# Kernel optimization log

Measured on AMD Instinct MI355X. Metric: run time of the kernel, lower is better.

The kernel has to match this reference:

```python
import jax, jax.numpy as jnp
import numpy as np

B, H, N, D, E = 2, 8, 512, 16, 128  # batch, heads, nodes, qkv_dim, embedding_dim


def setup_inputs() -> dict:
    key = jax.random.key(0)
    ks = jax.random.split(key, 6)
    return {
        "q": jax.random.normal(ks[0], (B, H, N, D), dtype=jnp.float32),
        "k": jax.random.normal(ks[1], (B, H, N, D), dtype=jnp.float32),
        "v": jax.random.normal(ks[2], (B, H, N, D), dtype=jnp.float32),
        "z": jax.random.normal(ks[3], (B, N, N, E), dtype=jnp.float32),
        "Wz1": jax.random.normal(ks[4], (E, H * D), dtype=jnp.float32) * (1.0 / np.sqrt(E)),
        "Wz2": jax.random.normal(ks[5], (E, H * D), dtype=jnp.float32) * (1.0 / np.sqrt(E)),
    }


def _heads(zp, b, n, h):
    # [b, n, n, h*d] -> [b, h, n, n, d]
    return zp.reshape(b, n, n, h, -1).transpose(0, 3, 1, 2, 4)


def reference(q, k, v, z, Wz1, Wz2):
    b, h, n, d = q.shape
    z1 = _heads(z @ Wz1, b, n, h)  # bhnmd
    z2 = _heads(z @ Wz2, b, n, h)  # bhnmd
    # score = sum_d (q + z1) * (k + z2), expanded to avoid materializing qz/kz
    score = (jnp.einsum('bhnd,bhmd->bhnm', q, k)
             + jnp.einsum('bhnd,bhnmd->bhnm', q, z2)
             + jnp.einsum('bhnmd,bhmd->bhnm', z1, k)
             + jnp.einsum('bhnmd,bhnmd->bhnm', z1, z2))
    score = score / jnp.sqrt(jnp.asarray(d, dtype=score.dtype))
    weights = jax.nn.softmax(score, axis=-1)  # [b, h, n, m]
    out = jnp.einsum('bhnm,bhmd->bhnd', weights, v)
    return out.transpose(0, 2, 1, 3).reshape(b, n, h * d)
```

## Files before the change

kernel.cpp:

```cpp
#include <hip/hip_runtime.h>

constexpr int CB = 2;
constexpr int CH = 8;
constexpr int CN = 512;
constexpr int CD = 16;
constexpr int CE = 128;
constexpr int CHD = CH * CD;
constexpr int TM = 32;
constexpr int NTILE = CN / TM;
constexpr int NT = 512;

typedef __attribute__((ext_vector_type(8))) short short8;
typedef __attribute__((ext_vector_type(4))) float f32x4;

__device__ __forceinline__ unsigned short f2bf_rne(float x) {
  union { float f; unsigned int u; } a; a.f = x;
  unsigned int r = a.u + 0x7fffu + ((a.u >> 16) & 1u);
  return (unsigned short)(r >> 16);
}

__device__ __forceinline__ void split_pair(float x0, float x1,
                                           unsigned int& hi, unsigned int& lo) {
  unsigned int u0 = __float_as_uint(x0), u1 = __float_as_uint(x1);
  unsigned int h0 = u0 & 0xffff0000u, h1 = u1 & 0xffff0000u;
  float l0 = x0 - __uint_as_float(h0);
  float l1 = x1 - __uint_as_float(h1);
  hi = h1 | (u0 >> 16);
  lo = (__float_as_uint(l1) & 0xffff0000u) | (__float_as_uint(l0) >> 16);
}

__device__ __forceinline__ void split8(const float4 a, const float4 b,
                                       short8& hi, short8& lo) {
  union { unsigned int u[4]; short8 s; } H, L;
  split_pair(a.x, a.y, H.u[0], L.u[0]);
  split_pair(a.z, a.w, H.u[1], L.u[1]);
  split_pair(b.x, b.y, H.u[2], L.u[2]);
  split_pair(b.z, b.w, H.u[3], L.u[3]);
  hi = H.s; lo = L.s;
}

#define MFMA(A, B, C) __builtin_amdgcn_mfma_f32_16x16x32_bf16((A), (B), (C), 0, 0, 0)

__global__ __launch_bounds__(NT, 4) void fused_mixedscore_attn(
    const float* __restrict__ q, const float* __restrict__ kk,
    const float* __restrict__ v, const float* __restrict__ z,
    const float* __restrict__ W1, const float* __restrict__ W2,
    float* __restrict__ out)
{
  const int n = blockIdx.x;
  const int b = blockIdx.y;
  const int tid = threadIdx.x;
  const int lane = tid & 63;
  const int h = tid >> 6;
  const int col = lane & 15;
  const int quad = lane >> 4;

  __shared__ unsigned short zh[2][TM * CE];
  __shared__ unsigned short zl[2][TM * CE];

  const float* gz = z + (size_t)(b * CN + n) * CN * CE;

  const int sr = tid >> 4;
  const int sc = (tid & 15) * 8;
  const int wb = sr * 256 + ((sc * 2) ^ ((sr & 7) << 4));

  float4 zr0, zr1;
  {
    const float* g0 = gz + sr * CE + sc;
    zr0 = *(const float4*)(g0);
    zr1 = *(const float4*)(g0 + 4);
  }

  short8 B1[4], B2[4];
  {
    const int c = h * CD + col;
#pragma unroll
    for (int ks = 0; ks < 4; ++ks) {
      union { unsigned int u[4]; short8 s; } U1, U2;
#pragma unroll
      for (int jp = 0; jp < 4; ++jp) {
        const int e = ks * 32 + quad * 8 + jp * 2;
        const float a0 = W1[(size_t)e * CHD + c];
        const float a1 = W1[(size_t)(e + 1) * CHD + c];
        const float w0 = W2[(size_t)e * CHD + c];
        const float w1 = W2[(size_t)(e + 1) * CHD + c];
        U1.u[jp] = (unsigned int)f2bf_rne(a0) | ((unsigned int)f2bf_rne(a1) << 16);
        U2.u[jp] = (unsigned int)f2bf_rne(w0) | ((unsigned int)f2bf_rne(w1) << 16);
      }
      B1[ks] = U1.s;
      B2[ks] = U2.s;
    }
  }

  const float4 qv =
      *(const float4*)&q[((size_t)(b * CH + h) * CN + n) * CD + quad * 4];

  f32x4 Oa = f32x4{0.f, 0.f, 0.f, 0.f};
  float mrun = -3.0e38f;
  float srun = 0.f;

  for (int t = 0; t < NTILE; ++t) {
    const int cb = t & 1;
    const int m0 = t * TM;

    {
      short8 h8, l8;
      split8(zr0, zr1, h8, l8);
      *(short8*)((char*)&zh[cb][0] + wb) = h8;
      *(short8*)((char*)&zl[cb][0] + wb) = l8;
    }
    __syncthreads();

    if (t + 1 < NTILE) {
      const float* g1 = gz + ((size_t)(t + 1) * TM + sr) * CE + sc;
      zr0 = *(const float4*)(g1);
      zr1 = *(const float4*)(g1 + 4);
    }

    f32x4 acc1[2], acc2[2];
#pragma unroll
    for (int mt = 0; mt < 2; ++mt) {
      acc1[mt] = f32x4{0.f, 0.f, 0.f, 0.f};
      acc2[mt] = f32x4{0.f, 0.f, 0.f, 0.f};
    }

    const char* zhb = (const char*)&zh[cb][0];
    const char* zlb = (const char*)&zl[cb][0];
#pragma unroll
    for (int ks = 0; ks < 4; ++ks) {
#pragma unroll
      for (int mt = 0; mt < 2; ++mt) {
        const int row = mt * 16 + col;
        const int off = row * 256 + ((ks * 64 + quad * 16) ^ ((row & 7) << 4));
        const short8 ah = *(const short8*)(zhb + off);
        const short8 al = *(const short8*)(zlb + off);
        acc1[mt] = MFMA(B1[ks], ah, acc1[mt]);
        acc2[mt] = MFMA(B2[ks], ah, acc2[mt]);
        acc1[mt] = MFMA(B1[ks], al, acc1[mt]);
        acc2[mt] = MFMA(B2[ks], al, acc2[mt]);
      }
    }

    float sc2[2];
#pragma unroll
    for (int mt = 0; mt < 2; ++mt) {
      const int m = m0 + mt * 16 + col;
      const float4 k4 =
          *(const float4*)&kk[((size_t)(b * CH + h) * CN + m) * CD + quad * 4];
      float p = (qv.x + acc1[mt][0]) * (k4.x + acc2[mt][0]);
      p += (qv.y + acc1[mt][1]) * (k4.y + acc2[mt][1]);
      p += (qv.z + acc1[mt][2]) * (k4.z + acc2[mt][2]);
      p += (qv.w + acc1[mt][3]) * (k4.w + acc2[mt][3]);
      p += __shfl_xor(p, 16);
      p += __shfl_xor(p, 32);
      sc2[mt] = p * 0.25f;
    }

    {
      float tmax = fmaxf(sc2[0], sc2[1]);
      tmax = fmaxf(tmax, __shfl_xor(tmax, 1));
      tmax = fmaxf(tmax, __shfl_xor(tmax, 2));
      tmax = fmaxf(tmax, __shfl_xor(tmax, 4));
      tmax = fmaxf(tmax, __shfl_xor(tmax, 8));
      const float mnew = fmaxf(mrun, tmax);
      const float alpha = __expf(mrun - mnew);
      mrun = mnew;
      const float e0 = __expf(sc2[0] - mnew);
      const float e1 = __expf(sc2[1] - mnew);
      float ls = e0 + e1;
      ls += __shfl_xor(ls, 1);
      ls += __shfl_xor(ls, 2);
      ls += __shfl_xor(ls, 4);
      ls += __shfl_xor(ls, 8);
      srun = srun * alpha + ls;

      const float* vb = v + ((size_t)(b * CH + h) * CN) * CD + quad * 4;
      const float4 v0 = *(const float4*)&vb[(size_t)(m0 + col) * CD];
      const float4 v1 = *(const float4*)&vb[(size_t)(m0 + 16 + col) * CD];
      Oa[0] = Oa[0] * alpha + e0 * v0.x + e1 * v1.x;
      Oa[1] = Oa[1] * alpha + e0 * v0.y + e1 * v1.y;
      Oa[2] = Oa[2] * alpha + e0 * v0.z + e1 * v1.z;
      Oa[3] = Oa[3] * alpha + e0 * v0.w + e1 * v1.w;
    }
  }

#pragma unroll
  for (int rg = 0; rg < 4; ++rg) {
    float o = Oa[rg];
    o += __shfl_xor(o, 1);
    o += __shfl_xor(o, 2);
    o += __shfl_xor(o, 4);
    o += __shfl_xor(o, 8);
    Oa[rg] = o;
  }
  if (col == 0) {
    const float inv = 1.0f / srun;
    float4 o4;
    o4.x = Oa[0] * inv;
    o4.y = Oa[1] * inv;
    o4.z = Oa[2] * inv;
    o4.w = Oa[3] * inv;
    *(float4*)&out[(size_t)(b * CN + n) * CHD + h * CD + quad * 4] = o4;
  }
}

extern "C" void kernel_launch(void* const* d_in, const int* in_sizes, int n_in,
                              void* d_out, int out_size, void* d_ws, size_t ws_size,
                              hipStream_t stream) {
  const float* q  = (const float*)d_in[0];
  const float* kv = (const float*)d_in[1];
  const float* v  = (const float*)d_in[2];
  const float* z  = (const float*)d_in[3];
  const float* W1 = (const float*)d_in[4];
  const float* W2 = (const float*)d_in[5];
  float* out = (float*)d_out;
  (void)in_sizes; (void)n_in; (void)out_size; (void)d_ws; (void)ws_size;

  dim3 grid(CN, CB);
  hipLaunchKernelGGL(fused_mixedscore_attn, grid, dim3(NT), 0, stream,
                     q, kv, v, z, W1, W2, out);
}
```

Measured before the change: 376.8 us.

## Double m-tile size to 64 and prefetch k/v before the MFMA loop

Raises the z tile per iteration from 32 to 64 rows, so each thread stages 16 floats instead of 8 and each wave runs four m-subtiles per barrier. This halves the number of loop iterations and __syncthreads calls and gives more MFMA work per sync. k and v loads for the tile are also moved to the top of the iteration so their latency overlaps the LDS staging and MFMAs. In exchange, LDS use doubles (64 KB across the two buffers) and register pressure rises, which may reduce occupancy under launch_bounds(512,4).

New measurement: 404.0 us. 7.2% more time.

```diff
diff --git a/kernel.cpp b/kernel.cpp
--- a/kernel.cpp
+++ b/kernel.cpp
@@ -6,7 +6,7 @@
 constexpr int CD = 16;
 constexpr int CE = 128;
 constexpr int CHD = CH * CD;
-constexpr int TM = 32;
+constexpr int TM = 64;
 constexpr int NTILE = CN / TM;
 constexpr int NT = 512;
 
@@ -60,15 +60,18 @@
 
   const float* gz = z + (size_t)(b * CN + n) * CN * CE;
 
-  const int sr = tid >> 4;
-  const int sc = (tid & 15) * 8;
-  const int wb = sr * 256 + ((sc * 2) ^ ((sr & 7) << 4));
-
-  float4 zr0, zr1;
+  const int sr = tid >> 3;
+  const int sc = (tid & 7) * 16;
+  const int wb0 = sr * 256 + ((sc * 2) ^ ((sr & 7) << 4));
+  const int wb1 = sr * 256 + ((sc * 2 + 16) ^ ((sr & 7) << 4));
+
+  float4 zr0, zr1, zr2, zr3;
   {
     const float* g0 = gz + sr * CE + sc;
     zr0 = *(const float4*)(g0);
     zr1 = *(const float4*)(g0 + 4);
+    zr2 = *(const float4*)(g0 + 8);
+    zr3 = *(const float4*)(g0 + 12);
   }
 
   short8 B1[4], B2[4];
@@ -99,15 +102,31 @@
   float mrun = -3.0e38f;
   float srun = 0.f;
 
+  const float* kbase = kk + ((size_t)(b * CH + h) * CN) * CD + quad * 4;
+  const float* vbase = v + ((size_t)(b * CH + h) * CN) * CD + quad * 4;
+
   for (int t = 0; t < NTILE; ++t) {
     const int cb = t & 1;
     const int m0 = t * TM;
 
+    float4 k4[4], v4[4];
+#pragma unroll
+    for (int mt = 0; mt < 4; ++mt) {
+      const size_t m = (size_t)(m0 + mt * 16 + col) * CD;
+      k4[mt] = *(const float4*)&kbase[m];
+      v4[mt] = *(const float4*)&vbase[m];
+    }
+
     {
+      char* zhb = (char*)&zh[cb][0];
+      char* zlb = (char*)&zl[cb][0];
       short8 h8, l8;
       split8(zr0, zr1, h8, l8);
-      *(short8*)((char*)&zh[cb][0] + wb) = h8;
-      *(short8*)((char*)&zl[cb][0] + wb) = l8;
+      *(short8*)(zhb + wb0) = h8;
+      *(short8*)(zlb + wb0) = l8;
+      split8(zr2, zr3, h8, l8);
+      *(short8*)(zhb + wb1) = h8;
+      *(short8*)(zlb + wb1) = l8;
     }
     __syncthreads();
 
@@ -115,11 +134,13 @@
       const float* g1 = gz + ((size_t)(t + 1) * TM + sr) * CE + sc;
       zr0 = *(const float4*)(g1);
       zr1 = *(const float4*)(g1 + 4);
-    }
-
-    f32x4 acc1[2], acc2[2];
-#pragma unroll
-    for (int mt = 0; mt < 2; ++mt) {
+      zr2 = *(const float4*)(g1 + 8);
+      zr3 = *(const float4*)(g1 + 12);
+    }
+
+    f32x4 acc1[4], acc2[4];
+#pragma unroll
+    for (int mt = 0; mt < 4; ++mt) {
       acc1[mt] = f32x4{0.f, 0.f, 0.f, 0.f};
       acc2[mt] = f32x4{0.f, 0.f, 0.f, 0.f};
     }
@@ -129,7 +150,7 @@
 #pragma unroll
     for (int ks = 0; ks < 4; ++ks) {
 #pragma unroll
-      for (int mt = 0; mt < 2; ++mt) {
+      for (int mt = 0; mt < 4; ++mt) {
         const int row = mt * 16 + col;
         const int off = row * 256 + ((ks * 64 + quad * 16) ^ ((row & 7) << 4));
         const short8 ah = *(const short8*)(zhb + off);
@@ -141,23 +162,20 @@
       }
     }
 
-    float sc2[2];
-#pragma unroll
-    for (int mt = 0; mt < 2; ++mt) {
-      const int m = m0 + mt * 16 + col;
-      const float4 k4 =
-          *(const float4*)&kk[((size_t)(b * CH + h) * CN + m) * CD + quad * 4];
-      float p = (qv.x + acc1[mt][0]) * (k4.x + acc2[mt][0]);
-      p += (qv.y + acc1[mt][1]) * (k4.y + acc2[mt][1]);
-      p += (qv.z + acc1[mt][2]) * (k4.z + acc2[mt][2]);
-      p += (qv.w + acc1[mt][3]) * (k4.w + acc2[mt][3]);
+    float sc2[4];
+#pragma unroll
+    for (int mt = 0; mt < 4; ++mt) {
+      float p = (qv.x + acc1[mt][0]) * (k4[mt].x + acc2[mt][0]);
+      p += (qv.y + acc1[mt][1]) * (k4[mt].y + acc2[mt][1]);
+      p += (qv.z + acc1[mt][2]) * (k4[mt].z + acc2[mt][2]);
+      p += (qv.w + acc1[mt][3]) * (k4[mt].w + acc2[mt][3]);
       p += __shfl_xor(p, 16);
       p += __shfl_xor(p, 32);
       sc2[mt] = p * 0.25f;
     }
 
     {
-      float tmax = fmaxf(sc2[0], sc2[1]);
+      float tmax = fmaxf(fmaxf(sc2[0], sc2[1]), fmaxf(sc2[2], sc2[3]));
       tmax = fmaxf(tmax, __shfl_xor(tmax, 1));
       tmax = fmaxf(tmax, __shfl_xor(tmax, 2));
       tmax = fmaxf(tmax, __shfl_xor(tmax, 4));
@@ -165,22 +183,31 @@
       const float mnew = fmaxf(mrun, tmax);
       const float alpha = __expf(mrun - mnew);
       mrun = mnew;
-      const float e0 = __expf(sc2[0] - mnew);
-      const float e1 = __expf(sc2[1] - mnew);
-      float ls = e0 + e1;
+      float e[4];
+      float ls = 0.f;
+#pragma unroll
+      for (int mt = 0; mt < 4; ++mt) {
+        e[mt] = __expf(sc2[mt] - mnew);
+        ls += e[mt];
+      }
       ls += __shfl_xor(ls, 1);
       ls += __shfl_xor(ls, 2);
       ls += __shfl_xor(ls, 4);
       ls += __shfl_xor(ls, 8);
       srun = srun * alpha + ls;
 
-      const float* vb = v + ((size_t)(b * CH + h) * CN) * CD + quad * 4;
-      const float4 v0 = *(const float4*)&vb[(size_t)(m0 + col) * CD];
-      const float4 v1 = *(const float4*)&vb[(size_t)(m0 + 16 + col) * CD];
-      Oa[0] = Oa[0] * alpha + e0 * v0.x + e1 * v1.x;
-      Oa[1] = Oa[1] * alpha + e0 * v0.y + e1 * v1.y;
-      Oa[2] = Oa[2] * alpha + e0 * v0.z + e1 * v1.z;
-      Oa[3] = Oa[3] * alpha + e0 * v0.w + e1 * v1.w;
+      float px = 0.f, py = 0.f, pz = 0.f, pw = 0.f;
+#pragma unroll
+      for (int mt = 0; mt < 4; ++mt) {
+        px += e[mt] * v4[mt].x;
+        py += e[mt] * v4[mt].y;
+        pz += e[mt] * v4[mt].z;
+        pw += e[mt] * v4[mt].w;
+      }
+      Oa[0] = Oa[0] * alpha + px;
+      Oa[1] = Oa[1] * alpha + py;
+      Oa[2] = Oa[2] * alpha + pz;
+      Oa[3] = Oa[3] * alpha + pw;
     }
   }
 
```

## Deepen z prefetch to two tiles and hoist k/v loads before MFMA

Applied to the files above, without the earlier changes.

The main loop is unrolled by two with separate register sets for the A and B tiles, so global loads of z run two tiles ahead instead of one. The k and v loads are moved to the start of each compute step so their latency overlaps the MFMA work. __syncthreads is replaced by an explicit lgkmcnt wait plus s_barrier, so outstanding global loads are not waited on at the barrier. This raises register pressure under launch bounds of 4 blocks, and the raw barrier relies on the wait covering LDS ordering.

After: 389.5 us. +3.4%, slower.

```diff
diff --git a/kernel.cpp b/kernel.cpp
--- a/kernel.cpp
+++ b/kernel.cpp
@@ -64,11 +64,14 @@
   const int sc = (tid & 15) * 8;
   const int wb = sr * 256 + ((sc * 2) ^ ((sr & 7) << 4));
 
-  float4 zr0, zr1;
+  float4 zA0, zA1, zB0, zB1;
   {
-    const float* g0 = gz + sr * CE + sc;
-    zr0 = *(const float4*)(g0);
-    zr1 = *(const float4*)(g0 + 4);
+    const float* gA = gz + sr * CE + sc;
+    zA0 = *(const float4*)(gA);
+    zA1 = *(const float4*)(gA + 4);
+    const float* gB = gz + ((size_t)TM + sr) * CE + sc;
+    zB0 = *(const float4*)(gB);
+    zB1 = *(const float4*)(gB + 4);
   }
 
   short8 B1[4], B2[4];
@@ -99,22 +102,23 @@
   float mrun = -3.0e38f;
   float srun = 0.f;
 
-  for (int t = 0; t < NTILE; ++t) {
-    const int cb = t & 1;
-    const int m0 = t * TM;
-
-    {
-      short8 h8, l8;
-      split8(zr0, zr1, h8, l8);
-      *(short8*)((char*)&zh[cb][0] + wb) = h8;
-      *(short8*)((char*)&zl[cb][0] + wb) = l8;
-    }
-    __syncthreads();
-
-    if (t + 1 < NTILE) {
-      const float* g1 = gz + ((size_t)(t + 1) * TM + sr) * CE + sc;
-      zr0 = *(const float4*)(g1);
-      zr1 = *(const float4*)(g1 + 4);
+  const float* kbase = kk + ((size_t)(b * CH + h) * CN) * CD + quad * 4;
+  const float* vbase = v + ((size_t)(b * CH + h) * CN) * CD + quad * 4;
+
+  auto stage = [&](int cb, const float4& r0, const float4& r1) {
+    short8 h8, l8;
+    split8(r0, r1, h8, l8);
+    *(short8*)((char*)&zh[cb][0] + wb) = h8;
+    *(short8*)((char*)&zl[cb][0] + wb) = l8;
+  };
+
+  auto compute = [&](int m0, int cb) {
+    float4 k4[2], v4[2];
+#pragma unroll
+    for (int mt = 0; mt < 2; ++mt) {
+      const size_t moff = (size_t)(m0 + mt * 16 + col) * CD;
+      k4[mt] = *(const float4*)&kbase[moff];
+      v4[mt] = *(const float4*)&vbase[moff];
     }
 
     f32x4 acc1[2], acc2[2];
@@ -144,44 +148,58 @@
     float sc2[2];
 #pragma unroll
     for (int mt = 0; mt < 2; ++mt) {
-      const int m = m0 + mt * 16 + col;
-      const float4 k4 =
-          *(const float4*)&kk[((size_t)(b * CH + h) * CN + m) * CD + quad * 4];
-      float p = (qv.x + acc1[mt][0]) * (k4.x + acc2[mt][0]);
-      p += (qv.y + acc1[mt][1]) * (k4.y + acc2[mt][1]);
-      p += (qv.z + acc1[mt][2]) * (k4.z + acc2[mt][2]);
-      p += (qv.w + acc1[mt][3]) * (k4.w + acc2[mt][3]);
+      float p = (qv.x + acc1[mt][0]) * (k4[mt].x + acc2[mt][0]);
+      p += (qv.y + acc1[mt][1]) * (k4[mt].y + acc2[mt][1]);
+      p += (qv.z + acc1[mt][2]) * (k4[mt].z + acc2[mt][2]);
+      p += (qv.w + acc1[mt][3]) * (k4[mt].w + acc2[mt][3]);
       p += __shfl_xor(p, 16);
       p += __shfl_xor(p, 32);
       sc2[mt] = p * 0.25f;
     }
 
-    {
-      float tmax = fmaxf(sc2[0], sc2[1]);
-      tmax = fmaxf(tmax, __shfl_xor(tmax, 1));
-      tmax = fmaxf(tmax, __shfl_xor(tmax, 2));
-      tmax = fmaxf(tmax, __shfl_xor(tmax, 4));
-      tmax = fmaxf(tmax, __shfl_xor(tmax, 8));
-      const float mnew = fmaxf(mrun, tmax);
-      const float alpha = __expf(mrun - mnew);
-      mrun = mnew;
-      const float e0 = __expf(sc2[0] - mnew);
-      const float e1 = __expf(sc2[1] - mnew);
-      float ls = e0 + e1;
-      ls += __shfl_xor(ls, 1);
-      ls += __shfl_xor(ls, 2);
-      ls += __shfl_xor(ls, 4);
-      ls += __shfl_xor(ls, 8);
-      srun = srun * alpha + ls;
-
-      const float* vb = v + ((size_t)(b * CH + h) * CN) * CD + quad * 4;
-      const float4 v0 = *(const float4*)&vb[(size_t)(m0 + col) * CD];
-      const float4 v1 = *(const float4*)&vb[(size_t)(m0 + 16 + col) * CD];
-      Oa[0] = Oa[0] * alpha + e0 * v0.x + e1 * v1.x;
-      Oa[1] = Oa[1] * alpha + e0 * v0.y + e1 * v1.y;
-      Oa[2] = Oa[2] * alpha + e0 * v0.z + e1 * v1.z;
-      Oa[3] = Oa[3] * alpha + e0 * v0.w + e1 * v1.w;
-    }
+    float tmax = fmaxf(sc2[0], sc2[1]);
+    tmax = fmaxf(tmax, __shfl_xor(tmax, 1));
+    tmax = fmaxf(tmax, __shfl_xor(tmax, 2));
+    tmax = fmaxf(tmax, __shfl_xor(tmax, 4));
+    tmax = fmaxf(tmax, __shfl_xor(tmax, 8));
+    const float mnew = fmaxf(mrun, tmax);
+    const float alpha = __expf(mrun - mnew);
+    mrun = mnew;
+    const float e0 = __expf(sc2[0] - mnew);
+    const float e1 = __expf(sc2[1] - mnew);
+    float ls = e0 + e1;
+    ls += __shfl_xor(ls, 1);
+    ls += __shfl_xor(ls, 2);
+    ls += __shfl_xor(ls, 4);
+    ls += __shfl_xor(ls, 8);
+    srun = srun * alpha + ls;
+
+    Oa[0] = Oa[0] * alpha + e0 * v4[0].x + e1 * v4[1].x;
+    Oa[1] = Oa[1] * alpha + e0 * v4[0].y + e1 * v4[1].y;
+    Oa[2] = Oa[2] * alpha + e0 * v4[0].z + e1 * v4[1].z;
+    Oa[3] = Oa[3] * alpha + e0 * v4[0].w + e1 * v4[1].w;
+  };
+
+  for (int tt = 0; tt < NTILE; tt += 2) {
+    stage(0, zA0, zA1);
+    asm volatile("s_waitcnt lgkmcnt(0)" ::: "memory");
+    __builtin_amdgcn_s_barrier();
+    if (tt + 2 < NTILE) {
+      const float* g = gz + ((size_t)(tt + 2) * TM + sr) * CE + sc;
+      zA0 = *(const float4*)(g);
+      zA1 = *(const float4*)(g + 4);
+    }
+    compute(tt * TM, 0);
+
+    stage(1, zB0, zB1);
+    asm volatile("s_waitcnt lgkmcnt(0)" ::: "memory");
+    __builtin_amdgcn_s_barrier();
+    if (tt + 3 < NTILE) {
+      const float* g = gz + ((size_t)(tt + 3) * TM + sr) * CE + sc;
+      zB0 = *(const float4*)(g);
+      zB1 = *(const float4*)(g + 4);
+    }
+    compute((tt + 1) * TM, 1);
   }
 
 #pragma unroll
```

## Remap waves to two heads by half-tile and add lazy softmax rescaling

Applied to the files above, without the earlier changes.

Each wave now handles two heads for one 16-row half of the z tile instead of one head for both halves. Every LDS A-fragment then feeds four head MFMAs (reused across two heads), halving shared-memory reads per MFMA. The online softmax switches to a per-half lazy max update that only rescales when a score exceeds the running max by more than 8, skipping most exp/rescale work. A shared-memory merge combines the two half-tile partial softmax states at the end. The launch-bounds occupancy hint drops from 4 to 2, giving more registers per thread for the doubled B fragments at the cost of fewer resident waves.

After: 412.8 us. +9.6%, slower.

```diff
diff --git a/kernel.cpp b/kernel.cpp
--- a/kernel.cpp
+++ b/kernel.cpp
@@ -41,7 +41,7 @@
 
 #define MFMA(A, B, C) __builtin_amdgcn_mfma_f32_16x16x32_bf16((A), (B), (C), 0, 0, 0)
 
-__global__ __launch_bounds__(NT, 4) void fused_mixedscore_attn(
+__global__ __launch_bounds__(NT, 2) void fused_mixedscore_attn(
     const float* __restrict__ q, const float* __restrict__ kk,
     const float* __restrict__ v, const float* __restrict__ z,
     const float* __restrict__ W1, const float* __restrict__ W2,
@@ -51,9 +51,13 @@
   const int b = blockIdx.y;
   const int tid = threadIdx.x;
   const int lane = tid & 63;
-  const int h = tid >> 6;
+  const int wave = tid >> 6;
+  const int g = wave >> 1;
+  const int half = wave & 1;
+  const int h0 = g * 2;
   const int col = lane & 15;
   const int quad = lane >> 4;
+  const int row = half * 16 + col;
 
   __shared__ unsigned short zh[2][TM * CE];
   __shared__ unsigned short zl[2][TM * CE];
@@ -61,19 +65,20 @@
   const float* gz = z + (size_t)(b * CN + n) * CN * CE;
 
   const int sr = tid >> 4;
-  const int sc = (tid & 15) * 8;
-  const int wb = sr * 256 + ((sc * 2) ^ ((sr & 7) << 4));
+  const int scf = (tid & 15) * 8;
+  const int wb = sr * 256 + ((scf * 2) ^ ((sr & 7) << 4));
 
   float4 zr0, zr1;
   {
-    const float* g0 = gz + sr * CE + sc;
+    const float* g0 = gz + sr * CE + scf;
     zr0 = *(const float4*)(g0);
     zr1 = *(const float4*)(g0 + 4);
   }
 
-  short8 B1[4], B2[4];
-  {
-    const int c = h * CD + col;
+  short8 B1[2][4], B2[2][4];
+#pragma unroll
+  for (int ct = 0; ct < 2; ++ct) {
+    const int c = (h0 + ct) * CD + col;
 #pragma unroll
     for (int ks = 0; ks < 4; ++ks) {
       union { unsigned int u[4]; short8 s; } U1, U2;
@@ -87,17 +92,23 @@
         U1.u[jp] = (unsigned int)f2bf_rne(a0) | ((unsigned int)f2bf_rne(a1) << 16);
         U2.u[jp] = (unsigned int)f2bf_rne(w0) | ((unsigned int)f2bf_rne(w1) << 16);
       }
-      B1[ks] = U1.s;
-      B2[ks] = U2.s;
-    }
-  }
-
-  const float4 qv =
-      *(const float4*)&q[((size_t)(b * CH + h) * CN + n) * CD + quad * 4];
-
-  f32x4 Oa = f32x4{0.f, 0.f, 0.f, 0.f};
-  float mrun = -3.0e38f;
-  float srun = 0.f;
+      B1[ct][ks] = U1.s;
+      B2[ct][ks] = U2.s;
+    }
+  }
+
+  float4 qv[2];
+  qv[0] = *(const float4*)&q[((size_t)(b * CH + h0) * CN + n) * CD + quad * 4];
+  qv[1] = *(const float4*)&q[((size_t)(b * CH + h0 + 1) * CN + n) * CD + quad * 4];
+
+  f32x4 Oa[2] = {f32x4{0.f, 0.f, 0.f, 0.f}, f32x4{0.f, 0.f, 0.f, 0.f}};
+  float mrun[2] = {-3.0e38f, -3.0e38f};
+  float srl[2] = {0.f, 0.f};
+
+  const float* kb0 = kk + ((size_t)(b * CH + h0) * CN) * CD + quad * 4;
+  const float* kb1 = kk + ((size_t)(b * CH + h0 + 1) * CN) * CD + quad * 4;
+  const float* vb0 = v + ((size_t)(b * CH + h0) * CN) * CD + quad * 4;
+  const float* vb1 = v + ((size_t)(b * CH + h0 + 1) * CN) * CD + quad * 4;
 
   for (int t = 0; t < NTILE; ++t) {
     const int cb = t & 1;
@@ -112,95 +123,118 @@
     __syncthreads();
 
     if (t + 1 < NTILE) {
-      const float* g1 = gz + ((size_t)(t + 1) * TM + sr) * CE + sc;
+      const float* g1 = gz + ((size_t)(t + 1) * TM + sr) * CE + scf;
       zr0 = *(const float4*)(g1);
       zr1 = *(const float4*)(g1 + 4);
     }
 
+    const size_t mo = (size_t)(m0 + row) * CD;
+    const float4 k40 = *(const float4*)&kb0[mo];
+    const float4 k41 = *(const float4*)&kb1[mo];
+    const float4 v40 = *(const float4*)&vb0[mo];
+    const float4 v41 = *(const float4*)&vb1[mo];
+
     f32x4 acc1[2], acc2[2];
 #pragma unroll
-    for (int mt = 0; mt < 2; ++mt) {
-      acc1[mt] = f32x4{0.f, 0.f, 0.f, 0.f};
-      acc2[mt] = f32x4{0.f, 0.f, 0.f, 0.f};
+    for (int ct = 0; ct < 2; ++ct) {
+      acc1[ct] = f32x4{0.f, 0.f, 0.f, 0.f};
+      acc2[ct] = f32x4{0.f, 0.f, 0.f, 0.f};
     }
 
     const char* zhb = (const char*)&zh[cb][0];
     const char* zlb = (const char*)&zl[cb][0];
 #pragma unroll
     for (int ks = 0; ks < 4; ++ks) {
-#pragma unroll
-      for (int mt = 0; mt < 2; ++mt) {
-        const int row = mt * 16 + col;
-        const int off = row * 256 + ((ks * 64 + quad * 16) ^ ((row & 7) << 4));
-        const short8 ah = *(const short8*)(zhb + off);
-        const short8 al = *(const short8*)(zlb + off);
-        acc1[mt] = MFMA(B1[ks], ah, acc1[mt]);
-        acc2[mt] = MFMA(B2[ks], ah, acc2[mt]);
-        acc1[mt] = MFMA(B1[ks], al, acc1[mt]);
-        acc2[mt] = MFMA(B2[ks], al, acc2[mt]);
-      }
-    }
-
-    float sc2[2];
-#pragma unroll
-    for (int mt = 0; mt < 2; ++mt) {
-      const int m = m0 + mt * 16 + col;
-      const float4 k4 =
-          *(const float4*)&kk[((size_t)(b * CH + h) * CN + m) * CD + quad * 4];
-      float p = (qv.x + acc1[mt][0]) * (k4.x + acc2[mt][0]);
-      p += (qv.y + acc1[mt][1]) * (k4.y + acc2[mt][1]);
-      p += (qv.z + acc1[mt][2]) * (k4.z + acc2[mt][2]);
-      p += (qv.w + acc1[mt][3]) * (k4.w + acc2[mt][3]);
+      const int off = row * 256 + ((ks * 64 + quad * 16) ^ ((row & 7) << 4));
+      const short8 ah = *(const short8*)(zhb + off);
+      const short8 al = *(const short8*)(zlb + off);
+      acc1[0] = MFMA(B1[0][ks], ah, acc1[0]);
+      acc1[1] = MFMA(B1[1][ks], ah, acc1[1]);
+      acc2[0] = MFMA(B2[0][ks], ah, acc2[0]);
+      acc2[1] = MFMA(B2[1][ks], ah, acc2[1]);
+      acc1[0] = MFMA(B1[0][ks], al, acc1[0]);
+      acc1[1] = MFMA(B1[1][ks], al, acc1[1]);
+      acc2[0] = MFMA(B2[0][ks], al, acc2[0]);
+      acc2[1] = MFMA(B2[1][ks], al, acc2[1]);
+    }
+
+#pragma unroll
+    for (int ct = 0; ct < 2; ++ct) {
+      const float4 k4 = ct ? k41 : k40;
+      const float4 v4 = ct ? v41 : v40;
+      float p = (qv[ct].x + acc1[ct][0]) * (k4.x + acc2[ct][0]);
+      p += (qv[ct].y + acc1[ct][1]) * (k4.y + acc2[ct][1]);
+      p += (qv[ct].z + acc1[ct][2]) * (k4.z + acc2[ct][2]);
+      p += (qv[ct].w + acc1[ct][3]) * (k4.w + acc2[ct][3]);
       p += __shfl_xor(p, 16);
       p += __shfl_xor(p, 32);
-      sc2[mt] = p * 0.25f;
-    }
-
-    {
-      float tmax = fmaxf(sc2[0], sc2[1]);
-      tmax = fmaxf(tmax, __shfl_xor(tmax, 1));
-      tmax = fmaxf(tmax, __shfl_xor(tmax, 2));
-      tmax = fmaxf(tmax, __shfl_xor(tmax, 4));
-      tmax = fmaxf(tmax, __shfl_xor(tmax, 8));
-      const float mnew = fmaxf(mrun, tmax);
-      const float alpha = __expf(mrun - mnew);
-      mrun = mnew;
-      const float e0 = __expf(sc2[0] - mnew);
-      const float e1 = __expf(sc2[1] - mnew);
-      float ls = e0 + e1;
-      ls += __shfl_xor(ls, 1);
-      ls += __shfl_xor(ls, 2);
-      ls += __shfl_xor(ls, 4);
-      ls += __shfl_xor(ls, 8);
-      srun = srun * alpha + ls;
-
-      const float* vb = v + ((size_t)(b * CH + h) * CN) * CD + quad * 4;
-      const float4 v0 = *(const float4*)&vb[(size_t)(m0 + col) * CD];
-      const float4 v1 = *(const float4*)&vb[(size_t)(m0 + 16 + col) * CD];
-      Oa[0] = Oa[0] * alpha + e0 * v0.x + e1 * v1.x;
-      Oa[1] = Oa[1] * alpha + e0 * v0.y + e1 * v1.y;
-      Oa[2] = Oa[2] * alpha + e0 * v0.z + e1 * v1.z;
-      Oa[3] = Oa[3] * alpha + e0 * v0.w + e1 * v1.w;
-    }
-  }
-
-#pragma unroll
-  for (int rg = 0; rg < 4; ++rg) {
-    float o = Oa[rg];
-    o += __shfl_xor(o, 1);
-    o += __shfl_xor(o, 2);
-    o += __shfl_xor(o, 4);
-    o += __shfl_xor(o, 8);
-    Oa[rg] = o;
-  }
-  if (col == 0) {
-    const float inv = 1.0f / srun;
-    float4 o4;
-    o4.x = Oa[0] * inv;
-    o4.y = Oa[1] * inv;
-    o4.z = Oa[2] * inv;
-    o4.w = Oa[3] * inv;
-    *(float4*)&out[(size_t)(b * CN + n) * CHD + h * CD + quad * 4] = o4;
+      const float s = p * 0.25f;
+
+      if (__any(s > mrun[ct] + 8.0f)) {
+        float tmax = s;
+        tmax = fmaxf(tmax, __shfl_xor(tmax, 1));
+        tmax = fmaxf(tmax, __shfl_xor(tmax, 2));
+        tmax = fmaxf(tmax, __shfl_xor(tmax, 4));
+        tmax = fmaxf(tmax, __shfl_xor(tmax, 8));
+        const float mnew = fmaxf(mrun[ct], tmax);
+        const float alpha = __expf(mrun[ct] - mnew);
+        srl[ct] *= alpha;
+        Oa[ct][0] *= alpha;
+        Oa[ct][1] *= alpha;
+        Oa[ct][2] *= alpha;
+        Oa[ct][3] *= alpha;
+        mrun[ct] = mnew;
+      }
+      const float e = __expf(s - mrun[ct]);
+      srl[ct] += e;
+      Oa[ct][0] += e * v4.x;
+      Oa[ct][1] += e * v4.y;
+      Oa[ct][2] += e * v4.z;
+      Oa[ct][3] += e * v4.w;
+    }
+  }
+
+  __syncthreads();
+  float* scratch = (float*)&zh[0][0];
+
+#pragma unroll
+  for (int ct = 0; ct < 2; ++ct) {
+    float S = srl[ct];
+    S += __shfl_xor(S, 1);
+    S += __shfl_xor(S, 2);
+    S += __shfl_xor(S, 4);
+    S += __shfl_xor(S, 8);
+    float o[4];
+#pragma unroll
+    for (int rg = 0; rg < 4; ++rg) {
+      float x = Oa[ct][rg];
+      x += __shfl_xor(x, 1);
+      x += __shfl_xor(x, 2);
+      x += __shfl_xor(x, 4);
+      x += __shfl_xor(x, 8);
+      o[rg] = x;
+    }
+    float* dst = scratch + ((h0 + ct) * 2 + half) * 20;
+    if (col == 0) {
+      dst[2 + quad * 4 + 0] = o[0];
+      dst[2 + quad * 4 + 1] = o[1];
+      dst[2 + quad * 4 + 2] = o[2];
+      dst[2 + quad * 4 + 3] = o[3];
+      if (quad == 0) { dst[0] = mrun[ct]; dst[1] = S; }
+    }
+  }
+  __syncthreads();
+
+  if (tid < CHD) {
+    const int h = tid >> 4, d = tid & 15;
+    const float* p0 = scratch + (h * 2 + 0) * 20;
+    const float* p1 = scratch + (h * 2 + 1) * 20;
+    const float m0v = p0[0], m1v = p1[0];
+    const float mm = fmaxf(m0v, m1v);
+    const float w0 = __expf(m0v - mm), w1 = __expf(m1v - mm);
+    const float Sv = p0[1] * w0 + p1[1] * w1;
+    const float Ov = p0[2 + d] * w0 + p1[2 + d] * w1;
+    out[(size_t)(b * CN + n) * CHD + h * CD + d] = Ov / Sv;
   }
 }
 
```
